# Kernel optimization log

Measured on AMD Instinct MI355X. Metric: run time of the kernel, lower is better.

## Reference

```python
import jax, jax.numpy as jnp
import numpy as np

B, L, D, P = 4, 128, 256, 1024
TU, TB = 86400, 3600  # tu = 24*3600, time_bin = 3600
NEG = float(-2**32 + 1)


def setup_inputs() -> dict:
    key = jax.random.key(0)
    ks = jax.random.split(key, 16)
    src = jax.random.normal(ks[0], (B, L, D), jnp.float32)
    batch_seq_lens = jax.random.randint(ks[1], (B,), L // 2, L + 1, dtype=jnp.int32)
    ts = jnp.sort(jax.random.randint(ks[2], (B, L), 0, 864000, dtype=jnp.int32), axis=1)
    lts = ts + jax.random.randint(ks[3], (B, L), 0, 7200, dtype=jnp.int32)
    s = 0.02
    hour_emb = (jax.random.normal(ks[4], (TU // TB + 2, D), jnp.float32) * s).at[0].set(0.0)  # padding_idx=0
    day_emb = (jax.random.normal(ks[5], (8, D), jnp.float32) * s).at[0].set(0.0)              # padding_idx=0
    wq = jax.random.normal(ks[6], (D, D), jnp.float32) * s
    wk = jax.random.normal(ks[7], (D, D), jnp.float32) * s
    wv = jax.random.normal(ks[8], (D, D), jnp.float32) * s
    wf1 = jax.random.normal(ks[9], (D, D), jnp.float32) * s
    wf2 = jax.random.normal(ks[10], (D, D), jnp.float32) * s
    wdec = jax.random.uniform(ks[11], (P, D), jnp.float32, -0.1, 0.1)  # init_weights uniform(-0.1,0.1)
    z = jnp.zeros((D,), jnp.float32)
    return {
        'src': src, 'hour_emb': hour_emb, 'day_emb': day_emb,
        'wq': wq, 'bq': z, 'wk': wk, 'bk': z, 'wv': wv, 'bv': z,
        'g11': jnp.ones((D,), jnp.float32), 'b11': z,
        'wf1': wf1, 'bf1': z, 'wf2': wf2, 'bf2': z,
        'g12': jnp.ones((D,), jnp.float32), 'b12': z,
        'wdec': wdec, 'bdec': jnp.zeros((P,), jnp.float32),
        'batch_seq_lens': batch_seq_lens,
        'batch_input_seqs_ts': ts,
        'batch_label_seqs_ts': lts,
    }


def _ln(x, g, b):
    m = jnp.mean(x, axis=-1, keepdims=True)
    v = jnp.var(x, axis=-1, keepdims=True)
    return (x - m) * jax.lax.rsqrt(v + 1e-5) * g + b


def reference(src, hour_emb, day_emb, wq, bq, wk, bk, wv, bv, g11, b11,
              wf1, bf1, wf2, bf2, g12, b12, wdec, bdec,
              batch_seq_lens, batch_input_seqs_ts, batch_label_seqs_ts):
    ts, lts = batch_input_seqs_ts, batch_label_seqs_ts
    # per-pair time intervals, [B,L,L]
    diff = ts[:, :, None] - ts[:, None, :]
    hour = (diff % TU) // TB + 2
    # faithful to source: 'if i == j' compares batch index to row position
    hour = jnp.where((jnp.arange(B)[:, None] == jnp.arange(L)[None, :])[:, :, None], 1, hour)
    day = jnp.minimum(diff // TU + 1, 7)
    ldiff = lts[:, :, None] - ts[:, None, :]
    lhour = (ldiff % TU) // TB + 2
    lday = jnp.minimum(ldiff // TU + 1, 7)
    tril = jnp.tril(jnp.ones((L, L), bool))
    rows_valid = jnp.arange(L)[None, :] < batch_seq_lens[:, None]  # [B,L]
    valid = tril[None] & rows_valid[:, :, None]
    # index 0 == padding row (zero embedding), matching zeros-init + padding_idx=0
    hour = jnp.where(valid, hour, 0)
    day = jnp.where(valid, day, 0)
    lhour = jnp.where(valid, lhour, 0)
    lday = jnp.where(valid, lday, 0)
    hE = hour_emb[hour]    # [B,L,L,D]
    dE = day_emb[day]
    lhE = hour_emb[lhour]
    ldE = day_emb[lday]

    Q = src @ wq.T + bq
    K = src @ wk.T + bk
    V = src @ wv.T + bv
    aw = (jnp.einsum('bjd,bkd->bjk', Q, K)
          + jnp.einsum('bjkd,bjd->bjk', hE, Q)
          + jnp.einsum('bjkd,bjd->bjk', dE, Q)) / jnp.sqrt(jnp.float32(D))
    mask = (~tril)[None] | (~rows_valid)[:, :, None]
    aw = jnp.where(mask, NEG, aw)
    aw = jax.nn.softmax(aw, axis=-1)
    x = (jnp.einsum('bjk,bkd->bjd', aw, V)
         + jnp.einsum('bjk,bjkd->bjd', aw, hE)
         + jnp.einsum('bjk,bjkd->bjd', aw, dE))
    x = _ln(x + src, g11, b11)
    f = jnp.maximum(x @ wf1.T + bf1, 0.0) @ wf2.T + bf2  # dropout is identity at eval
    f = _ln(x + f, g12, b12)

    # out4[b,j,k,:] = f[b,k,:] + label interval embeddings
    out4 = f[:, None, :, :] + lhE + ldE            # [B,L,L,D]
    dec = out4 @ wdec.T + bdec                     # [B,L,L,P]
    counts = jnp.arange(1, L + 1, dtype=dec.dtype)
    pooled = jnp.einsum('bjkp,jk->bjp', dec, tril.astype(dec.dtype)) / counts[None, :, None]
    return pooled
```

## Files before the change

kernel.cpp:

```cpp
#include <hip/hip_runtime.h>
#include <hip/hip_bf16.h>

#define LL 128
#define DD 256
#define PP 1024
#define TU_C 86400
#define TB_C 3600
#define NEGF -4294967296.0f

#define FMA4(ACC_, SS_, WW_) { (ACC_).x += (SS_)*(WW_).x; (ACC_).y += (SS_)*(WW_).y; (ACC_).z += (SS_)*(WW_).z; (ACC_).w += (SS_)*(WW_).w; }
#define ADD4(ACC_, WW_) { (ACC_).x += (WW_).x; (ACC_).y += (WW_).y; (ACC_).z += (WW_).z; (ACC_).w += (WW_).w; }

__device__ __forceinline__ float wredSum(float v) {
#pragma unroll
  for (int o = 32; o; o >>= 1) v += __shfl_xor(v, o);
  return v;
}
__device__ __forceinline__ float wredMax(float v) {
#pragma unroll
  for (int o = 32; o; o >>= 1) v = fmaxf(v, __shfl_xor(v, o));
  return v;
}

__global__ __launch_bounds__(256) void k_qkv2(
    const float* __restrict__ wq, const float* __restrict__ wk,
    const float* __restrict__ wv, const float* __restrict__ wf1,
    const float* __restrict__ wf2, const float* __restrict__ wdec,
    const float* __restrict__ src,
    const float* __restrict__ bq, const float* __restrict__ bk,
    const float* __restrict__ bv,
    float* __restrict__ WT,
    float* __restrict__ Q, float* __restrict__ KT, float* __restrict__ V)
{
  const int bx = blockIdx.x;
  const int t = threadIdx.x;
  if (bx >= 192) {
    __shared__ float s[32][33];
    const int tile = bx - 192;
    const float* sw; float* dst; int R, m;
    if (tile < 64)       { sw = wf1;  dst = WT + 196608; R = 256;  m = tile; }
    else if (tile < 128) { sw = wf2;  dst = WT + 262144; R = 256;  m = tile - 64; }
    else                 { sw = wdec; dst = WT + 327680; R = 1024; m = tile - 128; }
    const int sr = (m >> 3) * 32, sc0 = (m & 7) * 32;
    const int tx = t & 31, ty = t >> 5;
#pragma unroll
    for (int i = 0; i < 4; ++i)
      s[ty + 8 * i][tx] = sw[(sr + ty + 8 * i) * 256 + sc0 + tx];
    __syncthreads();
#pragma unroll
    for (int i = 0; i < 4; ++i)
      dst[(sc0 + ty + 8 * i) * R + sr + tx] = s[tx][ty + 8 * i];
    return;
  }
  const int mat = bx >> 6;
  const int r0 = (bx & 63) * 8;
  const float* wm = (mat == 0) ? wq : (mat == 1) ? wk : wv;
  __shared__ float xs[8][DD];
  __shared__ float wlds[16][260];
  for (int i = t; i < 8 * DD; i += 256) xs[i >> 8][i & 255] = src[r0 * DD + i];
  const int cg = t & 63, w = t >> 6;
  const int col4 = 4 * cg;
  const int rA = 2 * w, rB = rA + 1;
  float4 a0 = {0.f,0.f,0.f,0.f}, a1 = {0.f,0.f,0.f,0.f};
  for (int c = 0; c < 16; ++c) {
    const int e1 = c * 16;
    __syncthreads();
#pragma unroll
    for (int it = 0; it < 16; ++it) {
      const int idx = it * 256 + t;
      const int ccol = idx >> 4, eo = idx & 15;
      wlds[eo][ccol] = wm[ccol * 256 + e1 + eo];
    }
    __syncthreads();
#pragma unroll
    for (int eo = 0; eo < 16; ++eo) {
      const float4 w4 = *(const float4*)&wlds[eo][col4];
      FMA4(a0, xs[rA][e1 + eo], w4)
      FMA4(a1, xs[rB][e1 + eo], w4)
    }
  }
  const float* bi = (mat == 0) ? bq : (mat == 1) ? bk : bv;
  const float4 b4v = *(const float4*)(bi + col4);
  ADD4(a0, b4v) ADD4(a1, b4v)
  const int gA = r0 + rA, gB = r0 + rB;
  if (mat == 1) {
    const int bA = gA >> 7, kA = gA & 127;
    KT[bA * 32768 + (col4 + 0) * 128 + kA] = a0.x;
    KT[bA * 32768 + (col4 + 1) * 128 + kA] = a0.y;
    KT[bA * 32768 + (col4 + 2) * 128 + kA] = a0.z;
    KT[bA * 32768 + (col4 + 3) * 128 + kA] = a0.w;
    KT[bA * 32768 + (col4 + 0) * 128 + kA + 1] = a1.x;
    KT[bA * 32768 + (col4 + 1) * 128 + kA + 1] = a1.y;
    KT[bA * 32768 + (col4 + 2) * 128 + kA + 1] = a1.z;
    KT[bA * 32768 + (col4 + 3) * 128 + kA + 1] = a1.w;
  } else {
    float* o = (mat == 0) ? Q : V;
    *(float4*)(o + gA * DD + col4) = a0;
    *(float4*)(o + gB * DD + col4) = a1;
  }
}

__global__ __launch_bounds__(512) void k_attn(
    const float* __restrict__ Q, const float* __restrict__ KT,
    const float* __restrict__ Vm, const float* __restrict__ src,
    const float* __restrict__ hour_emb, const float* __restrict__ day_emb,
    const int* __restrict__ seq_lens, const int* __restrict__ ts_g,
    const float* __restrict__ g11, const float* __restrict__ b11,
    const float* __restrict__ wt1, const float* __restrict__ bf1,
    const float* __restrict__ wt2, const float* __restrict__ bf2,
    const float* __restrict__ g12, const float* __restrict__ b12,
    float* __restrict__ F)
{
  const int b = blockIdx.x >> 6;
  const int j0 = (blockIdx.x & 63) * 2;
  const int t = threadIdx.x, w = t >> 6, l = t & 63;
  const int col = 4 * l;
  __shared__ float qs[2][DD];
  __shared__ int   tsl[LL];
  __shared__ float qhd[2][34];
  __shared__ float whd[2][34];
  __shared__ float red[8];
  __shared__ float ss[2][LL];
  __shared__ float xs2[2][DD];
  __shared__ float hs2[2][DD];
  __shared__ float ps[8][2][DD];
  const int row0 = b * LL + j0;
  qs[t >> 8][t & 255] = Q[row0 * DD + t];
  if (t < LL) tsl[t] = ts_g[b * LL + t];
  if (t < 68) whd[t / 34][t % 34] = 0.f;
  __syncthreads();
  float kdot = 0.f;
  int krow = 0, kidx = 0;
  if (w < 4) {
    krow = w >> 1;
    kidx = ((w & 1) << 6) | l;
    const float* ktb = KT + b * 32768;
    float4 kd = {0.f,0.f,0.f,0.f};
#pragma unroll 8
    for (int e = 0; e < DD; e += 4) {
      const float4 q4 = *(const float4*)&qs[krow][e];
      const float* kp = ktb + e * LL + kidx;
      kd.x += q4.x * kp[0];
      kd.y += q4.y * kp[128];
      kd.z += q4.z * kp[256];
      kd.w += q4.w * kp[384];
    }
    kdot = (kd.x + kd.y) + (kd.z + kd.w);
  } else if (w < 6 && l < 34) {
    const int r = w - 4;
    const float* ep = (l < 26) ? (hour_emb + l * DD) : (day_emb + (l - 26) * DD);
    float4 ed = {0.f,0.f,0.f,0.f};
    for (int e = 0; e < DD; e += 4) {
      const float4 q4 = *(const float4*)&qs[r][e];
      const float4 e4 = *(const float4*)(ep + e);
      ed.x += q4.x * e4.x; ed.y += q4.y * e4.y;
      ed.z += q4.z * e4.z; ed.w += q4.w * e4.w;
    }
    qhd[r][l] = (ed.x + ed.y) + (ed.z + ed.w);
  }
  __syncthreads();
  const int len = seq_lens[b];
  float s = NEGF;
  int hidx = 0, didx = 0;
  if (w < 4) {
    const int jrow = j0 + krow;
    if (kidx <= jrow && jrow < len) {
      const int df = tsl[jrow] - tsl[kidx];
      hidx = (jrow == b) ? 1 : ((df % TU_C) / TB_C + 2);
      didx = min(df / TU_C + 1, 7);
      s = (kdot + qhd[krow][hidx] + qhd[krow][26 + didx]) * 0.0625f;
    }
    const float mv = wredMax(s);
    if (l == 0) red[w] = mv;
  }
  __syncthreads();
  float p = 0.f;
  if (w < 4) {
    const float m = fmaxf(red[2 * krow], red[2 * krow + 1]);
    p = expf(s - m);
    const float sv = wredSum(p);
    if (l == 0) red[4 + w] = sv;
  }
  __syncthreads();
  if (w < 4) {
    const float Z = red[4 + 2 * krow] + red[5 + 2 * krow];
    const float aw = p / Z;
    ss[krow][kidx] = aw;
    atomicAdd(&whd[krow][hidx], aw);
    atomicAdd(&whd[krow][26 + didx], aw);
  }
  __syncthreads();
  {
    float4 a0 = {0.f,0.f,0.f,0.f}, a1 = {0.f,0.f,0.f,0.f};
    const float* vb = Vm + b * LL * DD + col;
    const int k0 = 16 * w;
#pragma unroll
    for (int kk = 0; kk < 16; ++kk) {
      const int k = k0 + kk;
      const float4 v4 = *(const float4*)(vb + k * DD);
      FMA4(a0, ss[0][k], v4)
      FMA4(a1, ss[1][k], v4)
    }
    if (w == 0) {
#pragma unroll
      for (int i = 0; i < 26; ++i)
        FMA4(a0, whd[0][i], *(const float4*)(hour_emb + i * DD + col))
    } else if (w == 1) {
#pragma unroll
      for (int i = 0; i < 26; ++i)
        FMA4(a1, whd[1][i], *(const float4*)(hour_emb + i * DD + col))
    } else if (w == 2) {
#pragma unroll
      for (int i = 0; i < 8; ++i)
        FMA4(a0, whd[0][26 + i], *(const float4*)(day_emb + i * DD + col))
      const float4 s4 = *(const float4*)(src + row0 * DD + col);
      ADD4(a0, s4)
    } else if (w == 3) {
#pragma unroll
      for (int i = 0; i < 8; ++i)
        FMA4(a1, whd[1][26 + i], *(const float4*)(day_emb + i * DD + col))
      const float4 s4 = *(const float4*)(src + (row0 + 1) * DD + col);
      ADD4(a1, s4)
    }
    *(float4*)&ps[w][0][col] = a0;
    *(float4*)&ps[w][1][col] = a1;
  }
  __syncthreads();
  if (w < 2) {
    float4 x = *(const float4*)&ps[0][w][col];
#pragma unroll
    for (int i = 1; i < 8; ++i) ADD4(x, (*(const float4*)&ps[i][w][col]))
    const float sm = wredSum(x.x + x.y + x.z + x.w);
    const float sq = wredSum(x.x*x.x + x.y*x.y + x.z*x.z + x.w*x.w);
    const float mean = sm * (1.f / DD);
    const float rstd = rsqrtf(sq * (1.f / DD) - mean * mean + 1e-5f);
    const float4 g4 = *(const float4*)(g11 + col);
    const float4 b4 = *(const float4*)(b11 + col);
    x.x = (x.x - mean) * rstd * g4.x + b4.x;
    x.y = (x.y - mean) * rstd * g4.y + b4.y;
    x.z = (x.z - mean) * rstd * g4.z + b4.z;
    x.w = (x.w - mean) * rstd * g4.w + b4.w;
    *(float4*)&xs2[w][col] = x;
  }
  __syncthreads();
  {
    float4 a0 = {0.f,0.f,0.f,0.f}, a1 = {0.f,0.f,0.f,0.f};
    const int e0 = 32 * w;
#pragma unroll 8
    for (int ee = 0; ee < 32; ++ee) {
      const int e = e0 + ee;
      const float4 w4 = *(const float4*)(wt1 + e * DD + col);
      FMA4(a0, xs2[0][e], w4)
      FMA4(a1, xs2[1][e], w4)
    }
    *(float4*)&ps[w][0][col] = a0;
    *(float4*)&ps[w][1][col] = a1;
  }
  __syncthreads();
  if (w < 2) {
    float4 h = *(const float4*)(bf1 + col);
#pragma unroll
    for (int i = 0; i < 8; ++i) ADD4(h, (*(const float4*)&ps[i][w][col]))
    h.x = fmaxf(h.x, 0.f); h.y = fmaxf(h.y, 0.f);
    h.z = fmaxf(h.z, 0.f); h.w = fmaxf(h.w, 0.f);
    *(float4*)&hs2[w][col] = h;
  }
  __syncthreads();
  {
    float4 a0 = {0.f,0.f,0.f,0.f}, a1 = {0.f,0.f,0.f,0.f};
    const int e0 = 32 * w;
#pragma unroll 8
    for (int ee = 0; ee < 32; ++ee) {
      const int e = e0 + ee;
      const float4 w4 = *(const float4*)(wt2 + e * DD + col);
      FMA4(a0, hs2[0][e], w4)
      FMA4(a1, hs2[1][e], w4)
    }
    *(float4*)&ps[w][0][col] = a0;
    *(float4*)&ps[w][1][col] = a1;
  }
  __syncthreads();
  if (w < 2) {
    float4 o = *(const float4*)(bf2 + col);
#pragma unroll
    for (int i = 0; i < 8; ++i) ADD4(o, (*(const float4*)&ps[i][w][col]))
    const float4 xr = *(const float4*)&xs2[w][col];
    ADD4(o, xr)
    const float sm = wredSum(o.x + o.y + o.z + o.w);
    const float sq = wredSum(o.x*o.x + o.y*o.y + o.z*o.z + o.w*o.w);
    const float mean = sm * (1.f / DD);
    const float rstd = rsqrtf(sq * (1.f / DD) - mean * mean + 1e-5f);
    const float4 g4 = *(const float4*)(g12 + col);
    const float4 b4 = *(const float4*)(b12 + col);
    o.x = (o.x - mean) * rstd * g4.x + b4.x;
    o.y = (o.y - mean) * rstd * g4.y + b4.y;
    o.z = (o.z - mean) * rstd * g4.z + b4.z;
    o.w = (o.w - mean) * rstd * g4.w + b4.w;
    *(float4*)(F + (row0 + w) * DD + col) = o;
  }
}

__global__ __launch_bounds__(256) void k_decf(
    const float* __restrict__ F,
    const float* __restrict__ hour_emb, const float* __restrict__ day_emb,
    const int* __restrict__ seq_lens, const int* __restrict__ ts_g,
    const int* __restrict__ lts_g,
    const float* __restrict__ wtd, const float* __restrict__ bdec,
    float* __restrict__ out)
{
  const int c0 = blockIdx.x * 256;
  const int r0g = blockIdx.y * 8;
  const int b = r0g >> 7, j0 = r0g & 127;
  const int t = threadIdx.x, l = t & 63, w = t >> 6;
  __shared__ float xs[8][DD];
  __shared__ float cnt[8][34];
  __shared__ float ps[4][8][DD];
  for (int i = t; i < 8 * 34; i += 256) (&cnt[0][0])[i] = 0.f;
  __syncthreads();
  const int len = seq_lens[b];
  const int* ts = ts_g + b * LL;
  const int* lts = lts_g + b * LL;
#pragma unroll
  for (int p = 0; p < 4; ++p) {
    const int idx = p * 256 + t;
    const int jj = idx >> 7, k = idx & 127, j = j0 + jj;
    if (k <= j && j < len) {
      const int ld = lts[j] - ts[k];
      atomicAdd(&cnt[jj][(ld % TU_C) / TB_C + 2], 1.f);
      atomicAdd(&cnt[jj][26 + min(ld / TU_C + 1, 7)], 1.f);
    }
  }
  __syncthreads();
  {
    float he[26], de[8];
#pragma unroll
    for (int i = 0; i < 26; ++i) he[i] = hour_emb[i * DD + t];
#pragma unroll
    for (int i = 0; i < 8; ++i)  de[i] = day_emb[i * DD + t];
    const float* fb = F + b * LL * DD + t;
    float A0 = 0.f, A1 = 0.f, A2 = 0.f, A3 = 0.f;
#pragma unroll 4
    for (int k = 0; k < j0; k += 4) {
      A0 += fb[(k + 0) * DD]; A1 += fb[(k + 1) * DD];
      A2 += fb[(k + 2) * DD]; A3 += fb[(k + 3) * DD];
    }
    float gacc = (A0 + A1) + (A2 + A3);
#pragma unroll
    for (int jj = 0; jj < 8; ++jj) {
      gacc += fb[(j0 + jj) * DD];
      float s0 = 0.f, s1 = 0.f;
#pragma unroll
      for (int i = 0; i < 26; i += 2) {
        s0 += cnt[jj][i] * he[i]; s1 += cnt[jj][i + 1] * he[i + 1];
      }
#pragma unroll
      for (int i = 0; i < 8; i += 2) {
        s0 += cnt[jj][26 + i] * de[i]; s1 += cnt[jj][27 + i] * de[i + 1];
      }
      xs[jj][t] = (gacc + s0 + s1) / (float)(j0 + jj + 1);
    }
  }
  __syncthreads();
  const int col = c0 + 4 * l;
  float4 acc[8];
#pragma unroll
  for (int r = 0; r < 8; ++r) acc[r] = (float4){0.f, 0.f, 0.f, 0.f};
  const int e0 = 64 * w;
  for (int e = e0; e < e0 + 64; e += 4) {
    float4 xr[8];
#pragma unroll
    for (int r = 0; r < 8; ++r) xr[r] = *(const float4*)&xs[r][e];
#pragma unroll
    for (int c = 0; c < 4; ++c) {
      const float4 w4 = *(const float4*)(wtd + (e + c) * PP + col);
#pragma unroll
      for (int r = 0; r < 8; ++r) {
        const float xv = (c == 0) ? xr[r].x : (c == 1) ? xr[r].y : (c == 2) ? xr[r].z : xr[r].w;
        FMA4(acc[r], xv, w4)
      }
    }
  }
#pragma unroll
  for (int r = 0; r < 8; ++r) *(float4*)&ps[w][r][4 * l] = acc[r];
  __syncthreads();
#pragma unroll
  for (int g = 0; g < 2; ++g) {
    const int combo = g * 256 + t;
    const int r = combo >> 6, cgp = combo & 63;
    const int c4 = 4 * cgp;
    float4 o = *(const float4*)(bdec + c0 + c4);
    ADD4(o, (*(const float4*)&ps[0][r][c4]))
    ADD4(o, (*(const float4*)&ps[1][r][c4]))
    ADD4(o, (*(const float4*)&ps[2][r][c4]))
    ADD4(o, (*(const float4*)&ps[3][r][c4]))
    *(float4*)(out + (r0g + r) * PP + c0 + c4) = o;
  }
}

extern "C" void kernel_launch(void* const* d_in, const int* in_sizes, int n_in,
                              void* d_out, int out_size, void* d_ws, size_t ws_size,
                              hipStream_t stream)
{
  (void)in_sizes; (void)n_in; (void)out_size; (void)ws_size;
  const float* src      = (const float*)d_in[0];
  const float* hour_emb = (const float*)d_in[1];
  const float* day_emb  = (const float*)d_in[2];
  const float* wq  = (const float*)d_in[3];
  const float* bq  = (const float*)d_in[4];
  const float* wk  = (const float*)d_in[5];
  const float* bk  = (const float*)d_in[6];
  const float* wv  = (const float*)d_in[7];
  const float* bv  = (const float*)d_in[8];
  const float* g11 = (const float*)d_in[9];
  const float* b11 = (const float*)d_in[10];
  const float* wf1 = (const float*)d_in[11];
  const float* bf1 = (const float*)d_in[12];
  const float* wf2 = (const float*)d_in[13];
  const float* bf2 = (const float*)d_in[14];
  const float* g12 = (const float*)d_in[15];
  const float* b12 = (const float*)d_in[16];
  const float* wdec = (const float*)d_in[17];
  const float* bdec = (const float*)d_in[18];
  const int* seq_lens = (const int*)d_in[19];
  const int* ts  = (const int*)d_in[20];
  const int* lts = (const int*)d_in[21];
  float* out = (float*)d_out;
  float* ws = (float*)d_ws;
  float* WT = ws;
  float* Q  = ws + 589824;
  float* KT = ws + 720896;
  float* V  = ws + 851968;
  float* F  = ws + 983040;

  k_qkv2<<<576, 256, 0, stream>>>(wq, wk, wv, wf1, wf2, wdec, src,
                                  bq, bk, bv, WT, Q, KT, V);
  k_attn<<<256, 512, 0, stream>>>(Q, KT, V, src, hour_emb, day_emb, seq_lens, ts,
                                  g11, b11, WT + 196608, bf1, WT + 262144, bf2,
                                  g12, b12, F);
  k_decf<<<dim3(4, 64), 256, 0, stream>>>(F, hour_emb, day_emb, seq_lens, ts, lts,
                                          WT + 327680, bdec, out);
}
```

Baseline: 50.84 us.

## Fold weight-transpose tiles into QKV blocks, widen K chunk, merge softmax passes

Cuts the first kernel's grid from 576 to 256 blocks. Each of the 192 QKV blocks now also transposes one weight tile, and the 64 leftover blocks each transpose three tiles. The QKV inner loop loads 32-wide K chunks instead of 16, which halves the number of barrier rounds at the cost of more shared memory. In the attention kernel, the two-pass max/sum softmax becomes a single pass using an online-softmax rescale, removing one block-wide sync but adding extra expf calls.

```diff
diff --git a/kernel.cpp b/kernel.cpp
--- a/kernel.cpp
+++ b/kernel.cpp
@@ -34,46 +34,53 @@
 {
   const int bx = blockIdx.x;
   const int t = threadIdx.x;
-  if (bx >= 192) {
-    __shared__ float s[32][33];
-    const int tile = bx - 192;
+  __shared__ float xs[8][DD];
+  __shared__ float wlds[32][260];
+  __shared__ float st[32][33];
+
+  const int tx = t & 31, ty = t >> 5;
+  auto do_tile = [&](int tile) {
     const float* sw; float* dst; int R, m;
     if (tile < 64)       { sw = wf1;  dst = WT + 196608; R = 256;  m = tile; }
     else if (tile < 128) { sw = wf2;  dst = WT + 262144; R = 256;  m = tile - 64; }
     else                 { sw = wdec; dst = WT + 327680; R = 1024; m = tile - 128; }
     const int sr = (m >> 3) * 32, sc0 = (m & 7) * 32;
-    const int tx = t & 31, ty = t >> 5;
+    __syncthreads();
 #pragma unroll
     for (int i = 0; i < 4; ++i)
-      s[ty + 8 * i][tx] = sw[(sr + ty + 8 * i) * 256 + sc0 + tx];
+      st[ty + 8 * i][tx] = sw[(sr + ty + 8 * i) * 256 + sc0 + tx];
     __syncthreads();
 #pragma unroll
     for (int i = 0; i < 4; ++i)
-      dst[(sc0 + ty + 8 * i) * R + sr + tx] = s[tx][ty + 8 * i];
+      dst[(sc0 + ty + 8 * i) * R + sr + tx] = st[tx][ty + 8 * i];
+  };
+
+  if (bx >= 192) {
+#pragma unroll
+    for (int q = 0; q < 3; ++q) do_tile(192 + (bx - 192) * 3 + q);
     return;
   }
   const int mat = bx >> 6;
   const int r0 = (bx & 63) * 8;
   const float* wm = (mat == 0) ? wq : (mat == 1) ? wk : wv;
-  __shared__ float xs[8][DD];
-  __shared__ float wlds[16][260];
   for (int i = t; i < 8 * DD; i += 256) xs[i >> 8][i & 255] = src[r0 * DD + i];
+  do_tile(bx);
   const int cg = t & 63, w = t >> 6;
   const int col4 = 4 * cg;
   const int rA = 2 * w, rB = rA + 1;
   float4 a0 = {0.f,0.f,0.f,0.f}, a1 = {0.f,0.f,0.f,0.f};
-  for (int c = 0; c < 16; ++c) {
-    const int e1 = c * 16;
+  for (int c = 0; c < 8; ++c) {
+    const int e1 = c * 32;
     __syncthreads();
 #pragma unroll
-    for (int it = 0; it < 16; ++it) {
+    for (int it = 0; it < 32; ++it) {
       const int idx = it * 256 + t;
-      const int ccol = idx >> 4, eo = idx & 15;
+      const int ccol = idx >> 5, eo = idx & 31;
       wlds[eo][ccol] = wm[ccol * 256 + e1 + eo];
     }
     __syncthreads();
 #pragma unroll
-    for (int eo = 0; eo < 16; ++eo) {
+    for (int eo = 0; eo < 32; ++eo) {
       const float4 w4 = *(const float4*)&wlds[eo][col4];
       FMA4(a0, xs[rA][e1 + eo], w4)
       FMA4(a1, xs[rB][e1 + eo], w4)
@@ -162,6 +169,7 @@
   const int len = seq_lens[b];
   float s = NEGF;
   int hidx = 0, didx = 0;
+  float pv = 0.f, mw = 0.f;
   if (w < 4) {
     const int jrow = j0 + krow;
     if (kidx <= jrow && jrow < len) {
@@ -170,21 +178,18 @@
       didx = min(df / TU_C + 1, 7);
       s = (kdot + qhd[krow][hidx] + qhd[krow][26 + didx]) * 0.0625f;
     }
-    const float mv = wredMax(s);
-    if (l == 0) red[w] = mv;
-  }
-  __syncthreads();
-  float p = 0.f;
+    mw = wredMax(s);
+    pv = expf(s - mw);
+    const float zv = wredSum(pv);
+    if (l == 0) { red[w] = mw; red[4 + w] = zv; }
+  }
+  __syncthreads();
   if (w < 4) {
-    const float m = fmaxf(red[2 * krow], red[2 * krow + 1]);
-    p = expf(s - m);
-    const float sv = wredSum(p);
-    if (l == 0) red[4 + w] = sv;
-  }
-  __syncthreads();
-  if (w < 4) {
-    const float Z = red[4 + 2 * krow] + red[5 + 2 * krow];
-    const float aw = p / Z;
+    const float m0 = red[2 * krow], m1 = red[2 * krow + 1];
+    const float M = fmaxf(m0, m1);
+    const float Z = red[4 + 2 * krow] * expf(m0 - M)
+                  + red[5 + 2 * krow] * expf(m1 - M);
+    const float aw = pv * (expf(mw - M) / Z);
     ss[krow][kidx] = aw;
     atomicAdd(&whd[krow][hidx], aw);
     atomicAdd(&whd[krow][26 + didx], aw);
@@ -432,7 +437,7 @@
   float* V  = ws + 851968;
   float* F  = ws + 983040;
 
-  k_qkv2<<<576, 256, 0, stream>>>(wq, wk, wv, wf1, wf2, wdec, src,
+  k_qkv2<<<256, 256, 0, stream>>>(wq, wk, wv, wf1, wf2, wdec, src,
                                   bq, bk, bv, WT, Q, KT, V);
   k_attn<<<256, 512, 0, stream>>>(Q, KT, V, src, hour_emb, day_emb, seq_lens, ts,
                                   g11, b11, WT + 196608, bf1, WT + 262144, bf2,
```

Measured after the change: 53.22 us. +4.7%, slower.
